# Kernel tuning notes

Measured on AMD Instinct MI355X. Metric: run time of the kernel, lower is better.

## Reference

```python
import jax, jax.numpy as jnp
import numpy as np
import math

L, D, H, HD, F, G, V, P = 15, 512, 64, 8, 2048, 128, 7, 49
B, N = 4, 256


def setup_inputs() -> dict:
    key = jax.random.key(0)
    ks = jax.random.split(key, 24)
    nrm = lambda k, shape, s=0.02: (jax.random.normal(k, shape) * s).astype(jnp.float32)
    inp = {}
    inp["atom_types"] = jax.random.randint(ks[0], (B, N), 0, V)
    inp["coords"] = jax.random.normal(ks[1], (B, N, 3)) * 3.0
    inp["pair_types"] = jax.random.randint(ks[2], (B, N, N), 0, P)
    inp["mask"] = jnp.ones((B, N), dtype=bool)
    # embeddings / pair encoding params
    inp["atom_emb"] = nrm(ks[3], (V, D), 1.0).at[0].set(0.0)  # padding_idx=0
    inp["gaussian_mu"] = jax.random.normal(ks[4], (G,))
    inp["gaussian_sigma"] = jnp.ones((G,)) * 0.1
    inp["pair_a"] = jax.random.normal(ks[5], (P,)) * 0.01
    inp["pair_b"] = jax.random.normal(ks[6], (P,)) * 0.01
    inp["pl_w"] = nrm(ks[7], (G,))
    inp["pl_b"] = jnp.zeros(())
    # stacked per-layer params (leading dim L for lax.scan)
    inp["ln1_g"] = jnp.ones((L, D)); inp["ln1_b"] = jnp.zeros((L, D))
    inp["qkv_w"] = nrm(ks[8], (L, 3 * D, D)); inp["qkv_b"] = jnp.zeros((L, 3 * D))
    inp["pp_w"] = nrm(ks[9], (L, H), 0.1); inp["pp_b"] = jnp.zeros((L, H))
    inp["out_w"] = nrm(ks[10], (L, D, D)); inp["out_b"] = jnp.zeros((L, D))
    inp["ln2_g"] = jnp.ones((L, D)); inp["ln2_b"] = jnp.zeros((L, D))
    inp["ffn_w1"] = nrm(ks[11], (L, F, D)); inp["ffn_b1"] = jnp.zeros((L, F))
    inp["ffn_w2"] = nrm(ks[12], (L, D, F)); inp["ffn_b2"] = jnp.zeros((L, D))
    # SE3 head scalar affines (Linear(1,1) twice) and energy head
    inp["se3_uw"] = jnp.array(0.5); inp["se3_ub"] = jnp.array(0.01)
    inp["se3_ww"] = jnp.array(0.5); inp["se3_wb"] = jnp.array(0.01)
    inp["en_w"] = nrm(ks[13], (D,)); inp["en_b"] = jnp.zeros(())
    return inp


def _layernorm(x, g, b):
    m = x.mean(-1, keepdims=True)
    v = ((x - m) ** 2).mean(-1, keepdims=True)
    return (x - m) / jnp.sqrt(v + 1e-5) * g + b


def reference(atom_types, coords, pair_types, mask,
              atom_emb, gaussian_mu, gaussian_sigma, pair_a, pair_b, pl_w, pl_b,
              ln1_g, ln1_b, qkv_w, qkv_b, pp_w, pp_b, out_w, out_b,
              ln2_g, ln2_b, ffn_w1, ffn_b1, ffn_w2, ffn_b2,
              se3_uw, se3_ub, se3_ww, se3_wb, en_w, en_b):
    b_, n_ = atom_types.shape
    h = atom_emb[atom_types]  # [B,N,D]

    delta = coords[:, :, None, :] - coords[:, None, :, :]  # [B,N,N,3]
    d2 = (delta ** 2).sum(-1)
    dist = jnp.sqrt(jnp.maximum(d2, 1e-12))  # safe norm (grad-safe at 0)
    dist = jnp.where(mask[:, :, None], dist, 0.0)
    da = (pair_a[pair_types] * dist + pair_b[pair_types])[..., None]  # [B,N,N,1]
    gt = jnp.exp(-(da - gaussian_mu) ** 2) / (2.0 * gaussian_sigma ** 2)
    gt = gt / (gaussian_sigma * math.sqrt(2.0 * math.pi))
    gt = gt * mask[:, :, None, None]  # [B,N,N,G]
    pair_repr = gt @ pl_w + pl_b  # [B,N,N]
    pair_mask = mask[:, :, None] & mask[:, None, :]
    pair_repr = pair_repr * pair_mask

    scale = 1.0 / math.sqrt(HD)
    row_mask = mask[:, None, :, None]  # masks query rows, per original code

    def layer(hc, p):
        (l1g, l1b, qw, qb, ppw, ppb, ow, ob, l2g, l2b, w1, b1, w2, b2) = p
        x = _layernorm(hc, l1g, l1b)
        qkv = (x @ qw.T + qb).reshape(b_, n_, 3, H, HD)
        q, k, v = qkv[:, :, 0], qkv[:, :, 1], qkv[:, :, 2]
        scores = jnp.einsum('bnhd,bmhd->bhnm', q, k) * scale
        bias = pair_repr[..., None] * ppw + ppb  # [B,N,N,H]
        scores = scores + bias.transpose(0, 3, 1, 2)
        scores = jnp.where(row_mask, scores, -1e9)
        probs = jax.nn.softmax(scores, axis=-1)
        probs = jnp.where(jnp.isnan(probs), 0.0, probs)
        attn = jnp.einsum('bhnm,bmhd->bnhd', probs, v).reshape(b_, n_, D)
        hc = hc + attn @ ow.T + ob
        x2 = _layernorm(hc, l2g, l2b)
        ffn = jax.nn.gelu(x2 @ w1.T + b1, approximate=False) @ w2.T + b2
        return hc + ffn, None

    h, _ = jax.lax.scan(layer, h, (ln1_g, ln1_b, qkv_w, qkv_b, pp_w, pp_b,
                                   out_w, out_b, ln2_g, ln2_b,
                                   ffn_w1, ffn_b1, ffn_w2, ffn_b2))

    # --- SE3 equivariant head ---
    c = jax.nn.relu(pair_repr)[..., None]  # [B,N,N,1]
    c = c * se3_uw + se3_ub
    c = c * se3_ww + se3_wb
    c = c * mask[:, :, None, None]
    update = (delta * c).sum(axis=2)  # [B,N,3]
    num_valid = mask.sum(-1).astype(coords.dtype)[:, None, None] + 1e-6
    pred_coords = coords + update / num_valid

    cls = h[:, 0, :]
    pred_energy = cls @ en_w + en_b  # [B]
    return pred_coords, pred_energy


if __name__ == '__main__':
    out = reference(**setup_inputs())
    print(out[0].shape, out[1].shape)
```

## Files before the change

kernel.cpp:

```cpp
#include <hip/hip_runtime.h>
#include <hip/hip_bf16.h>
#include <math.h>

#define LAY 15
#define DIM 512
#define NH 64
#define HD 8
#define FF 2048
#define NG 128
#define BATCH 4
#define NTOK 256

typedef __attribute__((ext_vector_type(8))) short short8;
typedef __attribute__((ext_vector_type(4))) short short4v;
typedef __attribute__((ext_vector_type(8))) __bf16 bf16x8;
typedef __attribute__((ext_vector_type(4))) float f32x4;

__device__ inline short f2bs(float f) {
  __bf16 b = (__bf16)f;
  return __builtin_bit_cast(short, b);
}

__global__ __launch_bounds__(256) void embed_kernel(
    const int* __restrict__ types, const float* __restrict__ emb,
    float* __restrict__ h)
{
  int idx = blockIdx.x * 256 + threadIdx.x;
  int token = idx >> 9;
  int d = idx & 511;
  h[idx] = emb[types[token] * DIM + d];
}

__global__ __launch_bounds__(256) void cvt_all_kernel(
    const float* __restrict__ qkvw, const float* __restrict__ outw,
    const float* __restrict__ w1, const float* __restrict__ w2,
    short* __restrict__ dst)
{
  int i = blockIdx.x * 256 + threadIdx.x;
  const float* src;
  if (i < 1474560)      src = qkvw + (size_t)i * 8;
  else if (i < 1966080) src = outw + ((size_t)i - 1474560) * 8;
  else if (i < 3932160) src = w1 + ((size_t)i - 1966080) * 8;
  else                  src = w2 + ((size_t)i - 3932160) * 8;
  const float4* sp = (const float4*)src;
  float4 a = sp[0], b = sp[1];
  bf16x8 v;
  v[0] = (__bf16)a.x; v[1] = (__bf16)a.y; v[2] = (__bf16)a.z; v[3] = (__bf16)a.w;
  v[4] = (__bf16)b.x; v[5] = (__bf16)b.y; v[6] = (__bf16)b.z; v[7] = (__bf16)b.w;
  *(short8*)(dst + (size_t)i * 8) = __builtin_bit_cast(short8, v);
}

__global__ __launch_bounds__(256) void pair_kernel(
    const int* __restrict__ pair_types, const float* __restrict__ coords,
    const float* __restrict__ mu, const float* __restrict__ sigma,
    const float* __restrict__ pa, const float* __restrict__ pb,
    const float* __restrict__ plw, const float* __restrict__ plb,
    float* __restrict__ pair_repr)
{
  __shared__ float smu[NG], sw[NG];
  int tid = threadIdx.x;
  if (tid < NG) {
    float sg = sigma[tid];
    smu[tid] = mu[tid];
    sw[tid] = plw[tid] / (2.0f * sg * sg * sg * 2.5066282746310002f);
  }
  __syncthreads();
  int idx = blockIdx.x * 256 + tid;
  int b = idx >> 16;
  int ij = idx & 65535;
  int i = ij >> 8, j = ij & 255;
  const float* ci = coords + (b * NTOK + i) * 3;
  const float* cj = coords + (b * NTOK + j) * 3;
  float dx = ci[0] - cj[0], dy = ci[1] - cj[1], dz = ci[2] - cj[2];
  float d2 = dx * dx + dy * dy + dz * dz;
  float dist = sqrtf(fmaxf(d2, 1e-12f));
  int pt = pair_types[idx];
  float da = pa[pt] * dist + pb[pt];
  float acc = 0.0f;
#pragma unroll 8
  for (int g = 0; g < NG; ++g) {
    float t = da - smu[g];
    acc += __expf(-t * t) * sw[g];
  }
  pair_repr[idx] = acc + plb[0];
}

__global__ __launch_bounds__(256) void pairT_kernel(
    const float* __restrict__ pr, float* __restrict__ prT)
{
  __shared__ float tile[32][33];
  int b = blockIdx.z;
  int i0 = blockIdx.y * 32, j0 = blockIdx.x * 32;
  int tx = threadIdx.x & 31, ty = threadIdx.x >> 5;
#pragma unroll
  for (int r = 0; r < 4; ++r)
    tile[ty + r * 8][tx] = pr[((size_t)(b * NTOK + i0 + ty + r * 8)) * NTOK + j0 + tx];
  __syncthreads();
#pragma unroll
  for (int r = 0; r < 4; ++r)
    prT[((size_t)(b * NTOK + j0 + ty + r * 8)) * NTOK + i0 + tx] = tile[tx][ty + r * 8];
}

__global__ __launch_bounds__(256) void coord_kernel(
    const float* __restrict__ coords, const float* __restrict__ pair_repr,
    const float* __restrict__ uw, const float* __restrict__ ub,
    const float* __restrict__ ww, const float* __restrict__ wb,
    float* __restrict__ out)
{
  int bi = blockIdx.x;
  int b = bi >> 8;
  int j = threadIdx.x;
  float pr = pair_repr[bi * 256 + j];
  float c = fmaxf(pr, 0.0f);
  c = c * uw[0] + ub[0];
  c = c * ww[0] + wb[0];
  const float* ci = coords + bi * 3;
  const float* cj = coords + (b * NTOK + j) * 3;
  float sx = (ci[0] - cj[0]) * c;
  float sy = (ci[1] - cj[1]) * c;
  float sz = (ci[2] - cj[2]) * c;
#pragma unroll
  for (int o = 32; o > 0; o >>= 1) {
    sx += __shfl_xor(sx, o);
    sy += __shfl_xor(sy, o);
    sz += __shfl_xor(sz, o);
  }
  __shared__ float sm[4][3];
  if ((j & 63) == 0) {
    sm[j >> 6][0] = sx; sm[j >> 6][1] = sy; sm[j >> 6][2] = sz;
  }
  __syncthreads();
  if (j < 3) {
    float u = sm[0][j] + sm[1][j] + sm[2][j] + sm[3][j];
    out[bi * 3 + j] = coords[bi * 3 + j] + u * (1.0f / (256.0f + 1e-6f));
  }
}

__global__ __launch_bounds__(256) void ln_kernel(
    const float* __restrict__ h, const float* __restrict__ g,
    const float* __restrict__ beta, short* __restrict__ x)
{
  int t = blockIdx.x;
  int tid = threadIdx.x;
  const float* hp = h + t * DIM;
  float v0 = hp[tid], v1 = hp[tid + 256];
  __shared__ float sm[4];
  float s = v0 + v1;
#pragma unroll
  for (int o = 32; o > 0; o >>= 1) s += __shfl_xor(s, o);
  if ((tid & 63) == 0) sm[tid >> 6] = s;
  __syncthreads();
  float mean = (sm[0] + sm[1] + sm[2] + sm[3]) * (1.0f / 512.0f);
  float d0 = v0 - mean, d1 = v1 - mean;
  float ss = d0 * d0 + d1 * d1;
#pragma unroll
  for (int o = 32; o > 0; o >>= 1) ss += __shfl_xor(ss, o);
  __syncthreads();
  if ((tid & 63) == 0) sm[tid >> 6] = ss;
  __syncthreads();
  float var = (sm[0] + sm[1] + sm[2] + sm[3]) * (1.0f / 512.0f);
  float rstd = rsqrtf(var + 1e-5f);
  x[t * DIM + tid] = f2bs(d0 * rstd * g[tid] + beta[tid]);
  x[t * DIM + tid + 256] = f2bs(d1 * rstd * g[tid + 256] + beta[tid + 256]);
}

template <int MODE>
__global__ __launch_bounds__(128) void mm3(
    const short* __restrict__ A, const short* __restrict__ W,
    const float* __restrict__ bias, float* __restrict__ Cf,
    short* __restrict__ Cb, int N, int K, int kparts)
{
  __shared__ short As[2][2048];
  __shared__ short Bs[2][4096];
  int tid = threadIdx.x;
  int lane = tid & 63, wv = tid >> 6;
  int fr = lane & 15, fq = lane >> 4;
  int m0 = blockIdx.y * 32, n0 = blockIdx.x * 64;
  int Ksub = K / kparts;
  int kbeg = blockIdx.z * Ksub, kend = kbeg + Ksub;

  int arow[2], acol[2], brow[4], bcol[4];
#pragma unroll
  for (int r = 0; r < 2; ++r) {
    int id = r * 128 + tid;
    arow[r] = id >> 3;
    acol[r] = (id & 7) ^ (arow[r] & 7);
  }
#pragma unroll
  for (int r = 0; r < 4; ++r) {
    int id = r * 128 + tid;
    brow[r] = id >> 3;
    bcol[r] = (id & 7) ^ (brow[r] & 7);
  }

  auto stage = [&](int p, int k0) {
#pragma unroll
    for (int r = 0; r < 2; ++r) {
      const short* ga = &A[(size_t)(m0 + arow[r]) * K + k0 + acol[r] * 8];
      __builtin_amdgcn_global_load_lds(
          (const __attribute__((address_space(1))) void*)ga,
          (__attribute__((address_space(3))) void*)&As[p][(r * 128 + wv * 64) * 8],
          16, 0, 0);
    }
#pragma unroll
    for (int r = 0; r < 4; ++r) {
      const short* gw = &W[(size_t)(n0 + brow[r]) * K + k0 + bcol[r] * 8];
      __builtin_amdgcn_global_load_lds(
          (const __attribute__((address_space(1))) void*)gw,
          (__attribute__((address_space(3))) void*)&Bs[p][(r * 128 + wv * 64) * 8],
          16, 0, 0);
    }
  };

  f32x4 acc[2][2];
#pragma unroll
  for (int i = 0; i < 2; ++i)
#pragma unroll
    for (int j = 0; j < 2; ++j) acc[i][j] = (f32x4){0.f, 0.f, 0.f, 0.f};

  int aslot[2][2], bslot[2][2];
#pragma unroll
  for (int s = 0; s < 2; ++s)
#pragma unroll
    for (int i = 0; i < 2; ++i) {
      int m = i * 16 + fr;
      int c = s * 4 + fq;
      aslot[s][i] = m * 8 + (c ^ (m & 7));
      int n = wv * 32 + i * 16 + fr;
      bslot[s][i] = n * 8 + (c ^ (n & 7));
    }

  stage(0, kbeg);
  __syncthreads();
  int p = 0;
  for (int k0 = kbeg; k0 < kend; k0 += 64) {
    if (k0 + 64 < kend) stage(p ^ 1, k0 + 64);
    short8 af[2][2], bf_[2][2];
#pragma unroll
    for (int s = 0; s < 2; ++s)
#pragma unroll
      for (int i = 0; i < 2; ++i) {
        af[s][i] = *(const short8*)&As[p][aslot[s][i] * 8];
        bf_[s][i] = *(const short8*)&Bs[p][bslot[s][i] * 8];
      }
#pragma unroll
    for (int s = 0; s < 2; ++s)
#pragma unroll
      for (int i = 0; i < 2; ++i)
#pragma unroll
        for (int j = 0; j < 2; ++j)
          acc[i][j] = __builtin_amdgcn_mfma_f32_16x16x32_bf16(
              af[s][i], bf_[s][j], acc[i][j], 0, 0, 0);
    __syncthreads();
    p ^= 1;
  }

#pragma unroll
  for (int i = 0; i < 2; ++i) {
#pragma unroll
    for (int j = 0; j < 2; ++j) {
      int col = n0 + wv * 32 + j * 16 + fr;
      float bcol = bias[col];
#pragma unroll
      for (int rr = 0; rr < 4; ++rr) {
        int row = m0 + i * 16 + fq * 4 + rr;
        size_t idx = (size_t)row * N + col;
        float v = acc[i][j][rr];
        if (MODE == 1) {
          if (blockIdx.z == 0) v += bcol;
          atomicAdd(&Cf[idx], v);
        } else if (MODE == 2) {
          v += bcol;
          Cb[idx] = f2bs(0.5f * v * (1.0f + erff(v * 0.70710678118654752f)));
        } else {
          Cb[idx] = f2bs(v + bcol);
        }
      }
    }
  }
}

__global__ __launch_bounds__(128) void attn_mfma(
    const short* __restrict__ qkv, const float* __restrict__ prT,
    const float* __restrict__ ppw, const float* __restrict__ ppb,
    short* __restrict__ attn)
{
  __shared__ alignas(16) short Kl[256 * 8];
  __shared__ alignas(16) short Ql[128 * 8];
  __shared__ alignas(16) short VT[8 * 264];
  __shared__ alignas(16) short P[2 * 16 * 264];
  __shared__ alignas(16) float linv[32];
  int h = blockIdx.x, b = blockIdx.y;
  int qbase = blockIdx.z * 128;
  int tid = threadIdx.x;

#pragma unroll
  for (int r0 = 0; r0 < 2; ++r0) {
    int r = tid + r0 * 128;
    short8 kv = *(const short8*)&qkv[(size_t)(b * NTOK + r) * 1536 + 512 + h * 8];
    *(short8*)&Kl[r * 8] = kv;
    short8 vv = *(const short8*)&qkv[(size_t)(b * NTOK + r) * 1536 + 1024 + h * 8];
#pragma unroll
    for (int d = 0; d < 8; ++d) VT[d * 264 + r] = vv[d];
  }
  {
    short8 qv = *(const short8*)&qkv[(size_t)(b * NTOK + qbase + tid) * 1536 + h * 8];
    *(short8*)&Ql[tid * 8] = qv;
  }
  __syncthreads();

  int lane = tid & 63, w = tid >> 6;
  int fr = lane & 15, quad = lane >> 4;
  float pw = ppw[h], pbb = ppb[h];
  const float scale = 0.35355339059327373f;
  short8 zero8 = {0, 0, 0, 0, 0, 0, 0, 0};

  short8 vfrag[8];
#pragma unroll
  for (int kc = 0; kc < 8; ++kc)
    vfrag[kc] = (fr < 8) ? *(const short8*)&VT[fr * 264 + kc * 32 + quad * 8]
                         : zero8;

  short* Pw = &P[w * 16 * 264];
  float* lw = &linv[w * 16];

  for (int qt = 0; qt < 4; ++qt) {
    int qloc = w * 64 + qt * 16;
    int qg = qbase + qloc + fr;
    const float* prp = &prT[(size_t)b * 65536 + qg];
    float prv[16][4];
#pragma unroll
    for (int t = 0; t < 16; ++t)
#pragma unroll
      for (int r = 0; r < 4; ++r)
        prv[t][r] = prp[(size_t)(t * 16 + quad * 4 + r) * NTOK];

    short8 qf = zero8;
    if (quad == 0) qf = *(const short8*)&Ql[(qloc + fr) * 8];
    f32x4 sacc[16];
#pragma unroll
    for (int t = 0; t < 16; ++t) {
      short8 kf = zero8;
      if (quad == 0) kf = *(const short8*)&Kl[(t * 16 + fr) * 8];
      sacc[t] = __builtin_amdgcn_mfma_f32_16x16x32_bf16(
          kf, qf, (f32x4){0.f, 0.f, 0.f, 0.f}, 0, 0, 0);
    }

    float l = 0.f;
#pragma unroll
    for (int t = 0; t < 16; ++t) {
      short4v pk;
#pragma unroll
      for (int r = 0; r < 4; ++r) {
        float s = sacc[t][r] * scale + prv[t][r] * pw + pbb;
        float p = __expf(s);
        l += p;
        pk[r] = f2bs(p);
      }
      *(short4v*)&Pw[fr * 264 + t * 16 + quad * 4] = pk;
    }
    l += __shfl_xor(l, 16);
    l += __shfl_xor(l, 32);
    if (lane < 16) lw[fr] = 1.0f / l;

    f32x4 oacc = (f32x4){0.f, 0.f, 0.f, 0.f};
#pragma unroll
    for (int kc = 0; kc < 8; ++kc) {
      short8 pf = *(const short8*)&Pw[fr * 264 + kc * 32 + quad * 8];
      oacc = __builtin_amdgcn_mfma_f32_16x16x32_bf16(pf, vfrag[kc], oacc, 0, 0, 0);
    }
    if (fr < 8) {
      f32x4 li = *(f32x4*)&lw[quad * 4];
#pragma unroll
      for (int r = 0; r < 4; ++r) {
        int q = qbase + qloc + quad * 4 + r;
        attn[(size_t)(b * NTOK + q) * DIM + h * 8 + fr] = f2bs(oacc[r] * li[r]);
      }
    }
  }
}

__global__ __launch_bounds__(256) void energy_kernel(
    const float* __restrict__ h, const float* __restrict__ enw,
    const float* __restrict__ enb, float* __restrict__ out)
{
  int b = blockIdx.x;
  int tid = threadIdx.x;
  const float* hp = h + b * NTOK * DIM;
  float s = hp[tid] * enw[tid] + hp[tid + 256] * enw[tid + 256];
  __shared__ float sm[4];
#pragma unroll
  for (int o = 32; o > 0; o >>= 1) s += __shfl_xor(s, o);
  if ((tid & 63) == 0) sm[tid >> 6] = s;
  __syncthreads();
  if (tid == 0) out[BATCH * NTOK * 3 + b] = sm[0] + sm[1] + sm[2] + sm[3] + enb[0];
}

extern "C" void kernel_launch(void* const* d_in, const int* in_sizes, int n_in,
                              void* d_out, int out_size, void* d_ws, size_t ws_size,
                              hipStream_t stream)
{
  const int*   atom_types = (const int*)d_in[0];
  const float* coords     = (const float*)d_in[1];
  const int*   pair_types = (const int*)d_in[2];
  const float* atom_emb = (const float*)d_in[4];
  const float* gmu  = (const float*)d_in[5];
  const float* gsig = (const float*)d_in[6];
  const float* pa   = (const float*)d_in[7];
  const float* pb   = (const float*)d_in[8];
  const float* plw  = (const float*)d_in[9];
  const float* plb  = (const float*)d_in[10];
  const float* ln1g = (const float*)d_in[11];
  const float* ln1b = (const float*)d_in[12];
  const float* qkvw = (const float*)d_in[13];
  const float* qkvb = (const float*)d_in[14];
  const float* ppw  = (const float*)d_in[15];
  const float* ppb  = (const float*)d_in[16];
  const float* outw = (const float*)d_in[17];
  const float* outb = (const float*)d_in[18];
  const float* ln2g = (const float*)d_in[19];
  const float* ln2b = (const float*)d_in[20];
  const float* w1   = (const float*)d_in[21];
  const float* b1   = (const float*)d_in[22];
  const float* w2   = (const float*)d_in[23];
  const float* b2   = (const float*)d_in[24];
  const float* uw   = (const float*)d_in[25];
  const float* ub   = (const float*)d_in[26];
  const float* sww  = (const float*)d_in[27];
  const float* swb  = (const float*)d_in[28];
  const float* enw  = (const float*)d_in[29];
  const float* enb  = (const float*)d_in[30];

  float* out = (float*)d_out;
  float* ws  = (float*)d_ws;
  float* pair_repr = ws;
  float* prT  = pair_repr + 262144;
  float* h    = prT + 262144;
  short* qkv_bf  = (short*)(h + 524288);
  short* x_bf    = qkv_bf + 1572864;
  short* attn_bf = x_bf + 524288;
  short* ffn1_bf = attn_bf + 524288;
  short* qkvw_bf = ffn1_bf + 2097152;
  short* outw_bf = qkvw_bf + 11796480;
  short* w1_bf   = outw_bf + 3932160;
  short* w2_bf   = w1_bf + 15728640;

  cvt_all_kernel<<<23040, 256, 0, stream>>>(qkvw, outw, w1, w2, qkvw_bf);

  embed_kernel<<<2048, 256, 0, stream>>>(atom_types, atom_emb, h);
  pair_kernel<<<1024, 256, 0, stream>>>(pair_types, coords, gmu, gsig, pa, pb,
                                        plw, plb, pair_repr);
  pairT_kernel<<<dim3(8, 8, 4), 256, 0, stream>>>(pair_repr, prT);
  coord_kernel<<<1024, 256, 0, stream>>>(coords, pair_repr, uw, ub, sww, swb, out);

  for (int l = 0; l < LAY; ++l) {
    ln_kernel<<<1024, 256, 0, stream>>>(h, ln1g + l * DIM, ln1b + l * DIM, x_bf);
    mm3<3><<<dim3(24, 32, 1), 128, 0, stream>>>(
        x_bf, qkvw_bf + (size_t)l * 1536 * DIM, qkvb + l * 1536, nullptr, qkv_bf,
        1536, DIM, 1);
    attn_mfma<<<dim3(NH, BATCH, 2), 128, 0, stream>>>(
        qkv_bf, prT, ppw + l * NH, ppb + l * NH, attn_bf);
    mm3<1><<<dim3(8, 32, 2), 128, 0, stream>>>(
        attn_bf, outw_bf + (size_t)l * DIM * DIM, outb + l * DIM, h, nullptr,
        DIM, DIM, 2);
    ln_kernel<<<1024, 256, 0, stream>>>(h, ln2g + l * DIM, ln2b + l * DIM, x_bf);
    mm3<2><<<dim3(32, 32, 1), 128, 0, stream>>>(
        x_bf, w1_bf + (size_t)l * FF * DIM, b1 + l * FF, nullptr, ffn1_bf,
        FF, DIM, 1);
    mm3<1><<<dim3(8, 32, 4), 128, 0, stream>>>(
        ffn1_bf, w2_bf + (size_t)l * DIM * FF, b2 + l * DIM, h, nullptr,
        DIM, FF, 4);
  }
  energy_kernel<<<BATCH, 256, 0, stream>>>(h, enw, enb, out);
}
```

Before: 1.241 ms.

## Replace split-K atomics with partial buffers reduced in fused residual layernorm

Split-K GEMMs now write per-slice partial outputs to a workspace instead of atomically adding into the residual stream. A new layernorm kernel sums the partials into h before normalizing, and the energy head folds in the last layer's partials. The weight conversion kernel is also split into several launches that each convert 16 elements per thread. This removes atomic contention and nondeterminism at the cost of extra partial-buffer memory traffic.

```diff
diff --git a/kernel.cpp b/kernel.cpp
--- a/kernel.cpp
+++ b/kernel.cpp
@@ -10,6 +10,7 @@
 #define NG 128
 #define BATCH 4
 #define NTOK 256
+#define PSTRIDE 524288
 
 typedef __attribute__((ext_vector_type(8))) short short8;
 typedef __attribute__((ext_vector_type(4))) short short4v;
@@ -31,23 +32,26 @@
   h[idx] = emb[types[token] * DIM + d];
 }
 
-__global__ __launch_bounds__(256) void cvt_all_kernel(
+__global__ __launch_bounds__(256) void cvt2_kernel(
     const float* __restrict__ qkvw, const float* __restrict__ outw,
     const float* __restrict__ w1, const float* __restrict__ w2,
-    short* __restrict__ dst)
-{
-  int i = blockIdx.x * 256 + threadIdx.x;
-  const float* src;
-  if (i < 1474560)      src = qkvw + (size_t)i * 8;
-  else if (i < 1966080) src = outw + ((size_t)i - 1474560) * 8;
-  else if (i < 3932160) src = w1 + ((size_t)i - 1966080) * 8;
-  else                  src = w2 + ((size_t)i - 3932160) * 8;
-  const float4* sp = (const float4*)src;
-  float4 a = sp[0], b = sp[1];
-  bf16x8 v;
-  v[0] = (__bf16)a.x; v[1] = (__bf16)a.y; v[2] = (__bf16)a.z; v[3] = (__bf16)a.w;
-  v[4] = (__bf16)b.x; v[5] = (__bf16)b.y; v[6] = (__bf16)b.z; v[7] = (__bf16)b.w;
-  *(short8*)(dst + (size_t)i * 8) = __builtin_bit_cast(short8, v);
+    short* __restrict__ dst, int basePair)
+{
+  size_t i = ((size_t)basePair + blockIdx.x * 256 + threadIdx.x) * 2;
+  const float* src; size_t off;
+  if (i < 1474560)      { src = qkvw; off = i; }
+  else if (i < 1966080) { src = outw; off = i - 1474560; }
+  else if (i < 3932160) { src = w1;   off = i - 1966080; }
+  else                  { src = w2;   off = i - 3932160; }
+  const float4* sp = (const float4*)(src + off * 8);
+  float4 a = sp[0], b = sp[1], c = sp[2], d = sp[3];
+  bf16x8 v0, v1;
+  v0[0] = (__bf16)a.x; v0[1] = (__bf16)a.y; v0[2] = (__bf16)a.z; v0[3] = (__bf16)a.w;
+  v0[4] = (__bf16)b.x; v0[5] = (__bf16)b.y; v0[6] = (__bf16)b.z; v0[7] = (__bf16)b.w;
+  v1[0] = (__bf16)c.x; v1[1] = (__bf16)c.y; v1[2] = (__bf16)c.z; v1[3] = (__bf16)c.w;
+  v1[4] = (__bf16)d.x; v1[5] = (__bf16)d.y; v1[6] = (__bf16)d.z; v1[7] = (__bf16)d.w;
+  *(short8*)(dst + i * 8) = __builtin_bit_cast(short8, v0);
+  *(short8*)(dst + i * 8 + 8) = __builtin_bit_cast(short8, v1);
 }
 
 __global__ __launch_bounds__(256) void pair_kernel(
@@ -164,6 +168,41 @@
   x[t * DIM + tid + 256] = f2bs(d1 * rstd * g[tid + 256] + beta[tid + 256]);
 }
 
+__global__ __launch_bounds__(256) void ln_res_kernel(
+    float* __restrict__ h, const float* __restrict__ part, int kparts,
+    const float* __restrict__ g, const float* __restrict__ beta,
+    short* __restrict__ x)
+{
+  int t = blockIdx.x;
+  int tid = threadIdx.x;
+  size_t base = (size_t)t * DIM;
+  float v0 = h[base + tid], v1 = h[base + tid + 256];
+  for (int z = 0; z < kparts; ++z) {
+    v0 += part[(size_t)z * PSTRIDE + base + tid];
+    v1 += part[(size_t)z * PSTRIDE + base + tid + 256];
+  }
+  h[base + tid] = v0;
+  h[base + tid + 256] = v1;
+  __shared__ float sm[4];
+  float s = v0 + v1;
+#pragma unroll
+  for (int o = 32; o > 0; o >>= 1) s += __shfl_xor(s, o);
+  if ((tid & 63) == 0) sm[tid >> 6] = s;
+  __syncthreads();
+  float mean = (sm[0] + sm[1] + sm[2] + sm[3]) * (1.0f / 512.0f);
+  float d0 = v0 - mean, d1 = v1 - mean;
+  float ss = d0 * d0 + d1 * d1;
+#pragma unroll
+  for (int o = 32; o > 0; o >>= 1) ss += __shfl_xor(ss, o);
+  __syncthreads();
+  if ((tid & 63) == 0) sm[tid >> 6] = ss;
+  __syncthreads();
+  float var = (sm[0] + sm[1] + sm[2] + sm[3]) * (1.0f / 512.0f);
+  float rstd = rsqrtf(var + 1e-5f);
+  x[base + tid] = f2bs(d0 * rstd * g[tid] + beta[tid]);
+  x[base + tid + 256] = f2bs(d1 * rstd * g[tid + 256] + beta[tid + 256]);
+}
+
 template <int MODE>
 __global__ __launch_bounds__(128) void mm3(
     const short* __restrict__ A, const short* __restrict__ W,
@@ -266,14 +305,14 @@
         int row = m0 + i * 16 + fq * 4 + rr;
         size_t idx = (size_t)row * N + col;
         float v = acc[i][j][rr];
-        if (MODE == 1) {
-          if (blockIdx.z == 0) v += bcol;
-          atomicAdd(&Cf[idx], v);
-        } else if (MODE == 2) {
+        if (MODE == 2) {
           v += bcol;
           Cb[idx] = f2bs(0.5f * v * (1.0f + erff(v * 0.70710678118654752f)));
+        } else if (MODE == 3) {
+          Cb[idx] = f2bs(v + bcol);
         } else {
-          Cb[idx] = f2bs(v + bcol);
+          if (blockIdx.z == 0) v += bcol;
+          Cf[(size_t)blockIdx.z * PSTRIDE + idx] = v;
         }
       }
     }
@@ -381,13 +420,20 @@
 }
 
 __global__ __launch_bounds__(256) void energy_kernel(
-    const float* __restrict__ h, const float* __restrict__ enw,
-    const float* __restrict__ enb, float* __restrict__ out)
+    const float* __restrict__ h, const float* __restrict__ part,
+    const float* __restrict__ enw, const float* __restrict__ enb,
+    float* __restrict__ out)
 {
   int b = blockIdx.x;
   int tid = threadIdx.x;
-  const float* hp = h + b * NTOK * DIM;
-  float s = hp[tid] * enw[tid] + hp[tid + 256] * enw[tid + 256];
+  size_t base = (size_t)(b * NTOK) * DIM;
+  float x0 = h[base + tid], x1 = h[base + tid + 256];
+#pragma unroll
+  for (int z = 0; z < 4; ++z) {
+    x0 += part[(size_t)z * PSTRIDE + base + tid];
+    x1 += part[(size_t)z * PSTRIDE + base + tid + 256];
+  }
+  float s = x0 * enw[tid] + x1 * enw[tid + 256];
   __shared__ float sm[4];
 #pragma unroll
   for (int o = 32; o > 0; o >>= 1) s += __shfl_xor(s, o);
@@ -436,7 +482,8 @@
   float* pair_repr = ws;
   float* prT  = pair_repr + 262144;
   float* h    = prT + 262144;
-  short* qkv_bf  = (short*)(h + 524288);
+  float* part = h + 524288;
+  short* qkv_bf  = (short*)(part + 4 * 524288);
   short* x_bf    = qkv_bf + 1572864;
   short* attn_bf = x_bf + 524288;
   short* ffn1_bf = attn_bf + 524288;
@@ -445,7 +492,9 @@
   short* w1_bf   = outw_bf + 3932160;
   short* w2_bf   = w1_bf + 15728640;
 
-  cvt_all_kernel<<<23040, 256, 0, stream>>>(qkvw, outw, w1, w2, qkvw_bf);
+  for (int c = 0; c < 8; ++c)
+    cvt2_kernel<<<1440, 256, 0, stream>>>(qkvw, outw, w1, w2, qkvw_bf,
+                                          c * 368640);
 
   embed_kernel<<<2048, 256, 0, stream>>>(atom_types, atom_emb, h);
   pair_kernel<<<1024, 256, 0, stream>>>(pair_types, coords, gmu, gsig, pa, pb,
@@ -454,22 +503,27 @@
   coord_kernel<<<1024, 256, 0, stream>>>(coords, pair_repr, uw, ub, sww, swb, out);
 
   for (int l = 0; l < LAY; ++l) {
-    ln_kernel<<<1024, 256, 0, stream>>>(h, ln1g + l * DIM, ln1b + l * DIM, x_bf);
+    if (l == 0)
+      ln_kernel<<<1024, 256, 0, stream>>>(h, ln1g, ln1b, x_bf);
+    else
+      ln_res_kernel<<<1024, 256, 0, stream>>>(h, part, 4,
+                                              ln1g + l * DIM, ln1b + l * DIM, x_bf);
     mm3<3><<<dim3(24, 32, 1), 128, 0, stream>>>(
         x_bf, qkvw_bf + (size_t)l * 1536 * DIM, qkvb + l * 1536, nullptr, qkv_bf,
         1536, DIM, 1);
     attn_mfma<<<dim3(NH, BATCH, 2), 128, 0, stream>>>(
         qkv_bf, prT, ppw + l * NH, ppb + l * NH, attn_bf);
-    mm3<1><<<dim3(8, 32, 2), 128, 0, stream>>>(
-        attn_bf, outw_bf + (size_t)l * DIM * DIM, outb + l * DIM, h, nullptr,
+    mm3<4><<<dim3(8, 32, 2), 128, 0, stream>>>(
+        attn_bf, outw_bf + (size_t)l * DIM * DIM, outb + l * DIM, part, nullptr,
         DIM, DIM, 2);
-    ln_kernel<<<1024, 256, 0, stream>>>(h, ln2g + l * DIM, ln2b + l * DIM, x_bf);
+    ln_res_kernel<<<1024, 256, 0, stream>>>(h, part, 2,
+                                            ln2g + l * DIM, ln2b + l * DIM, x_bf);
     mm3<2><<<dim3(32, 32, 1), 128, 0, stream>>>(
         x_bf, w1_bf + (size_t)l * FF * DIM, b1 + l * FF, nullptr, ffn1_bf,
         FF, DIM, 1);
-    mm3<1><<<dim3(8, 32, 4), 128, 0, stream>>>(
-        ffn1_bf, w2_bf + (size_t)l * DIM * FF, b2 + l * DIM, h, nullptr,
+    mm3<4><<<dim3(8, 32, 4), 128, 0, stream>>>(
+        ffn1_bf, w2_bf + (size_t)l * DIM * FF, b2 + l * DIM, part, nullptr,
         DIM, FF, 4);
   }
-  energy_kernel<<<BATCH, 256, 0, stream>>>(h, enw, enb, out);
-}
+  energy_kernel<<<BATCH, 256, 0, stream>>>(h, part, enw, enb, out);
+}
```

Result: faster. 1.197 ms (-3.5%).
